# Kernel tuning notes

Measured on AMD Instinct MI355X. Metric: run time of the kernel, lower is better.

The kernel has to match this reference:

```python
import jax, jax.numpy as jnp
import numpy as np

B = 2097152   # batch
Z = 16        # z_dim
K = 64        # num_hidden_nodes


def setup_inputs() -> dict:
    key = jax.random.key(0)
    k1, k2, k3, k4, k5 = jax.random.split(key, 5)
    return {
        "z": jax.random.normal(k1, (B, Z), dtype=jnp.float32),
        "a_0": jax.random.normal(k2, (1,), dtype=jnp.float32),
        "bk": jax.random.normal(k3, (K,), dtype=jnp.float32),
        "ck": jax.random.normal(k4, (K, Z), dtype=jnp.float32),
        "dk": jax.random.normal(k5, (K,), dtype=jnp.float32),
    }


def reference(z, a_0, bk, ck, dk):
    # Vectorized over the batch: y[b] = a_0 + sum_k bk[k] * tanh((ck @ z[b])[k] + dk[k])
    h = jnp.tanh(jnp.einsum("bz,kz->bk", z, ck) + dk)  # [B, K]
    y = a_0 + h @ bk                                     # [B]
    return y[:, None]                                     # [B, 1]
```

## Files before the change

kernel.cpp:

```cpp
#include <hip/hip_runtime.h>
#include <stdint.h>

typedef __attribute__((ext_vector_type(8)))  short  short8;
typedef __attribute__((ext_vector_type(8)))  __bf16 bf16x8;
typedef __attribute__((ext_vector_type(16))) float  floatx16;
typedef __attribute__((ext_vector_type(4)))  float  floatx4;
typedef __attribute__((ext_vector_type(2)))  float  float2v;
typedef __attribute__((ext_vector_type(4)))  uint32_t uint4v;

union Frag { short8 s; bf16x8 v; uint4v d; };
union FU   { float f; uint32_t u; };

__device__ __forceinline__ short f2bf(float f) {
    FU x; x.f = f;
    uint32_t r = x.u + 0x7fffu + ((x.u >> 16) & 1u);
    return (short)(r >> 16);
}

__device__ __forceinline__ uint32_t pack_bf2(float lo, float hi) {
    FU a, b; a.f = lo; b.f = hi;
    return __builtin_amdgcn_perm(b.u + 0x8000u, a.u + 0x8000u, 0x07060302u);
}

__device__ __forceinline__ float fexp2(float x) { return __builtin_amdgcn_exp2f(x); }
__device__ __forceinline__ float frcp(float x)  { return __builtin_amdgcn_rcpf(x); }

__device__ __forceinline__ float2v tpair(float a, float b) {
    float2v t;
    t.x = fexp2(fminf(a, 15.0f));
    t.y = fexp2(fminf(b, 15.0f));
    return t + 1.0f;
}

__global__ __launch_bounds__(256, 7) void mave_kernel(
    const float* __restrict__ z,
    const float* __restrict__ a0,
    const float* __restrict__ bk,
    const float* __restrict__ ck,
    const float* __restrict__ dk,
    float* __restrict__ out,
    int ntiles)
{
    const int lane = threadIdx.x & 63;
    const int m    = lane & 31;
    const int g    = lane >> 5;
    const float S  = 2.885390081777927f;

    __shared__ __align__(16) float   cinitL[2][2][16];
    __shared__ __align__(16) float2v nbL[2][2][8];
    __shared__ float baseL;

    const int wid   = (int)((blockIdx.x * blockDim.x + threadIdx.x) >> 6);
    const int tile0 = wid * 4;
    const int tlast = ntiles - 1;

    const float* zp = z + (size_t)m * 16 + g * 8;

    floatx4 zb[2][2];
    #pragma unroll
    for (int i = 0; i < 2; ++i) {
        int ti = tile0 + i; if (ti > tlast) ti = tlast;
        const float* q = zp + (size_t)ti * 512;
        zb[i][0] = *(const floatx4*)q;
        zb[i][1] = *(const floatx4*)(q + 4);
    }

    Frag af[2];
    {
        const float* c0 = ck + m * 16 + g * 8;
        #pragma unroll
        for (int e = 0; e < 8; ++e) {
            af[0].s[e] = f2bf(c0[e] * S);
            af[1].s[e] = f2bf(c0[512 + e] * S);
        }
    }

    if (threadIdx.x < 64) {
        const int t = threadIdx.x;
        {
            const int gg = t >> 5, hh = (t >> 4) & 1, r = t & 15;
            const int n  = (r & 3) + 8 * (r >> 2) + 4 * gg + 32 * hh;
            cinitL[gg][hh][r] = S * dk[n];
        }
        if (t < 32) {
            const int gg = t >> 4, hh = (t >> 3) & 1, j = t & 7;
            const int nl = (j & 3) + 8 * (j >> 2) + 4 * gg + 32 * hh;
            float2v nb; nb.x = -2.0f * bk[nl]; nb.y = -2.0f * bk[nl + 16];
            nbL[gg][hh][j] = nb;
        }
        float bv = bk[t];
        #pragma unroll
        for (int d = 1; d < 64; d <<= 1) bv += __shfl_xor(bv, d, 64);
        if (t == 0) baseL = a0[0] + bv;
    }
    __syncthreads();

    if (tile0 >= ntiles) return;

    const floatx4* cqg = (const floatx4*)&cinitL[g][0][0];
    const floatx4* nqg = (const floatx4*)&nbL[g][0][0];

    float yv[4];
    #pragma unroll
    for (int i = 0; i < 4; ++i) {
        Frag bfr;
        bfr.d[0] = pack_bf2(zb[i & 1][0].x, zb[i & 1][0].y);
        bfr.d[1] = pack_bf2(zb[i & 1][0].z, zb[i & 1][0].w);
        bfr.d[2] = pack_bf2(zb[i & 1][1].x, zb[i & 1][1].y);
        bfr.d[3] = pack_bf2(zb[i & 1][1].z, zb[i & 1][1].w);

        if (i + 2 < 4) {
            int ti = tile0 + i + 2; if (ti > tlast) ti = tlast;
            const float* q = zp + (size_t)ti * 512;
            zb[i & 1][0] = *(const floatx4*)q;
            zb[i & 1][1] = *(const floatx4*)(q + 4);
        }

        int zz = 0;
        asm volatile("" : "+v"(zz));
        const floatx4* cq = cqg + zz;
        const floatx4* nq = nqg + zz;

        float ya = 0.0f;
        #pragma unroll
        for (int h = 0; h < 2; ++h) {
            union { floatx16 v; floatx4 q[4]; } C;
            C.q[0] = cq[h * 4 + 0]; C.q[1] = cq[h * 4 + 1];
            C.q[2] = cq[h * 4 + 2]; C.q[3] = cq[h * 4 + 3];
            floatx16 acc = __builtin_amdgcn_mfma_f32_32x32x16_bf16(
                af[h].v, bfr.v, C.v, 0, 0, 0);

            union { floatx4 q; float2v p[2]; } N0, N1, N2, N3;
            N0.q = nq[h * 4 + 0];
            N1.q = nq[h * 4 + 1];
            N2.q = nq[h * 4 + 2];
            N3.q = nq[h * 4 + 3];

            float2v T0 = tpair(acc[0], acc[8]);
            float2v T1 = tpair(acc[1], acc[9]);
            float2v P01 = T0 * T1;
            float2v n01 = N0.p[0] * T1 + N0.p[1] * T0;
            float2v T2 = tpair(acc[2], acc[10]);
            float2v T3 = tpair(acc[3], acc[11]);
            float2v P23 = T2 * T3;
            float2v n23 = N1.p[0] * T3 + N1.p[1] * T2;
            float2v T4 = tpair(acc[4], acc[12]);
            float2v T5 = tpair(acc[5], acc[13]);
            float2v P45 = T4 * T5;
            float2v n45 = N2.p[0] * T5 + N2.p[1] * T4;
            float2v T6 = tpair(acc[6], acc[14]);
            float2v T7 = tpair(acc[7], acc[15]);
            float2v P67 = T6 * T7;
            float2v n67 = N3.p[0] * T7 + N3.p[1] * T6;

            float2v PA = P01 * P23, PB = P45 * P67;
            float2v nA = n01 * P23 + n23 * P01;
            float2v nB = n45 * P67 + n67 * P45;
            float2v P  = PA * PB;
            float2v Num = nA * PB + nB * PA;
            float2v R; R.x = frcp(P.x); R.y = frcp(P.y);
            float2v Yh = Num * R;
            ya += Yh.x + Yh.y;
        }
        yv[i] = ya;
    }

    const float base = baseL;
    float ov[4];
    #pragma unroll
    for (int i = 0; i < 4; ++i) ov[i] = __shfl_xor(yv[i], 32, 64);
    if (g == 0) {
        #pragma unroll
        for (int i = 0; i < 4; ++i) {
            int ti = tile0 + i; if (ti > tlast) ti = tlast;
            out[(size_t)ti * 32 + m] = base + yv[i] + ov[i];
        }
    }
}

extern "C" void kernel_launch(void* const* d_in, const int* in_sizes, int n_in,
                              void* d_out, int out_size, void* d_ws, size_t ws_size,
                              hipStream_t stream) {
    const float* z  = (const float*)d_in[0];
    const float* a0 = (const float*)d_in[1];
    const float* bk = (const float*)d_in[2];
    const float* ck = (const float*)d_in[3];
    const float* dk = (const float*)d_in[4];
    float* out = (float*)d_out;

    const int B      = in_sizes[0] / 16;
    const int ntiles = B / 32;

    const int blocks = (ntiles + 15) / 16;
    hipLaunchKernelGGL(mave_kernel, dim3(blocks), dim3(256), 0, stream,
                       z, a0, bk, ck, dk, out, ntiles);
}
```

Measured before the change: 204.4 us.

## Give each wave private constant tables, drop block barrier, halve tiles per wave

Every wave now builds its own copy of the dk/bk-derived constant tables in shared memory and computes the bias sum itself. This removes the block-wide __syncthreads and the early-exit ordering around it. Each wave now handles two tiles instead of four, and the grid doubles to compensate. All loads, including ck, are issued up front so their latencies overlap. The cost is redundant per-wave setup work and more waves overall, with less amortization of that setup.

New measurement: 196.5 us. 3.9% less time.

```diff
diff --git a/kernel.cpp b/kernel.cpp
--- a/kernel.cpp
+++ b/kernel.cpp
@@ -44,18 +44,35 @@
     const int lane = threadIdx.x & 63;
     const int m    = lane & 31;
     const int g    = lane >> 5;
+    const int widx = threadIdx.x >> 6;
     const float S  = 2.885390081777927f;
 
-    __shared__ __align__(16) float   cinitL[2][2][16];
-    __shared__ __align__(16) float2v nbL[2][2][8];
-    __shared__ float baseL;
+    __shared__ __align__(16) float   cinitL[4][2][2][16];
+    __shared__ __align__(16) float2v nbL[4][2][2][8];
 
     const int wid   = (int)((blockIdx.x * blockDim.x + threadIdx.x) >> 6);
-    const int tile0 = wid * 4;
+    const int tile0 = wid * 2;
+    if (tile0 >= ntiles) return;
     const int tlast = ntiles - 1;
 
+    const float* c0 = ck + m * 16 + g * 8;
+    floatx4 ckv0 = *(const floatx4*)c0;
+    floatx4 ckv1 = *(const floatx4*)(c0 + 4);
+    floatx4 ckv2 = *(const floatx4*)(c0 + 512);
+    floatx4 ckv3 = *(const floatx4*)(c0 + 516);
+
+    const int tl = lane;
+    const int gg = tl >> 5, hh = (tl >> 4) & 1, rr = tl & 15;
+    const int nc = (rr & 3) + 8 * (rr >> 2) + 4 * gg + 32 * hh;
+    float dkv = dk[nc];
+    float bkt = bk[tl];
+    const int g2 = tl >> 4, h2 = (tl >> 3) & 1, j2 = tl & 7;
+    const int nl = (j2 & 3) + 8 * (j2 >> 2) + 4 * g2 + 32 * h2;
+    float bnl = 0.0f, bnh = 0.0f;
+    if (tl < 32) { bnl = bk[nl]; bnh = bk[nl + 16]; }
+    float a0v = a0[0];
+
     const float* zp = z + (size_t)m * 16 + g * 8;
-
     floatx4 zb[2][2];
     #pragma unroll
     for (int i = 0; i < 2; ++i) {
@@ -66,55 +83,35 @@
     }
 
     Frag af[2];
-    {
-        const float* c0 = ck + m * 16 + g * 8;
-        #pragma unroll
-        for (int e = 0; e < 8; ++e) {
-            af[0].s[e] = f2bf(c0[e] * S);
-            af[1].s[e] = f2bf(c0[512 + e] * S);
-        }
+    #pragma unroll
+    for (int e = 0; e < 4; ++e) {
+        af[0].s[e]     = f2bf(ckv0[e] * S);
+        af[0].s[e + 4] = f2bf(ckv1[e] * S);
+        af[1].s[e]     = f2bf(ckv2[e] * S);
+        af[1].s[e + 4] = f2bf(ckv3[e] * S);
     }
 
-    if (threadIdx.x < 64) {
-        const int t = threadIdx.x;
-        {
-            const int gg = t >> 5, hh = (t >> 4) & 1, r = t & 15;
-            const int n  = (r & 3) + 8 * (r >> 2) + 4 * gg + 32 * hh;
-            cinitL[gg][hh][r] = S * dk[n];
-        }
-        if (t < 32) {
-            const int gg = t >> 4, hh = (t >> 3) & 1, j = t & 7;
-            const int nl = (j & 3) + 8 * (j >> 2) + 4 * gg + 32 * hh;
-            float2v nb; nb.x = -2.0f * bk[nl]; nb.y = -2.0f * bk[nl + 16];
-            nbL[gg][hh][j] = nb;
-        }
-        float bv = bk[t];
-        #pragma unroll
-        for (int d = 1; d < 64; d <<= 1) bv += __shfl_xor(bv, d, 64);
-        if (t == 0) baseL = a0[0] + bv;
+    cinitL[widx][gg][hh][rr] = S * dkv;
+    if (tl < 32) {
+        float2v nb; nb.x = -2.0f * bnl; nb.y = -2.0f * bnh;
+        nbL[widx][g2][h2][j2] = nb;
     }
-    __syncthreads();
+    float bv = bkt;
+    #pragma unroll
+    for (int d = 1; d < 64; d <<= 1) bv += __shfl_xor(bv, d, 64);
+    const float base = a0v + bv;
 
-    if (tile0 >= ntiles) return;
+    const floatx4* cqg = (const floatx4*)&cinitL[widx][g][0][0];
+    const floatx4* nqg = (const floatx4*)&nbL[widx][g][0][0];
 
-    const floatx4* cqg = (const floatx4*)&cinitL[g][0][0];
-    const floatx4* nqg = (const floatx4*)&nbL[g][0][0];
-
-    float yv[4];
+    float yv[2];
     #pragma unroll
-    for (int i = 0; i < 4; ++i) {
+    for (int i = 0; i < 2; ++i) {
         Frag bfr;
-        bfr.d[0] = pack_bf2(zb[i & 1][0].x, zb[i & 1][0].y);
-        bfr.d[1] = pack_bf2(zb[i & 1][0].z, zb[i & 1][0].w);
-        bfr.d[2] = pack_bf2(zb[i & 1][1].x, zb[i & 1][1].y);
-        bfr.d[3] = pack_bf2(zb[i & 1][1].z, zb[i & 1][1].w);
-
-        if (i + 2 < 4) {
-            int ti = tile0 + i + 2; if (ti > tlast) ti = tlast;
-            const float* q = zp + (size_t)ti * 512;
-            zb[i & 1][0] = *(const floatx4*)q;
-            zb[i & 1][1] = *(const floatx4*)(q + 4);
-        }
+        bfr.d[0] = pack_bf2(zb[i][0].x, zb[i][0].y);
+        bfr.d[1] = pack_bf2(zb[i][0].z, zb[i][0].w);
+        bfr.d[2] = pack_bf2(zb[i][1].x, zb[i][1].y);
+        bfr.d[3] = pack_bf2(zb[i][1].z, zb[i][1].w);
 
         int zz = 0;
         asm volatile("" : "+v"(zz));
@@ -165,13 +162,12 @@
         yv[i] = ya;
     }
 
-    const float base = baseL;
-    float ov[4];
+    float ov[2];
     #pragma unroll
-    for (int i = 0; i < 4; ++i) ov[i] = __shfl_xor(yv[i], 32, 64);
+    for (int i = 0; i < 2; ++i) ov[i] = __shfl_xor(yv[i], 32, 64);
     if (g == 0) {
         #pragma unroll
-        for (int i = 0; i < 4; ++i) {
+        for (int i = 0; i < 2; ++i) {
             int ti = tile0 + i; if (ti > tlast) ti = tlast;
             out[(size_t)ti * 32 + m] = base + yv[i] + ov[i];
         }
@@ -191,7 +187,7 @@
     const int B      = in_sizes[0] / 16;
     const int ntiles = B / 32;
 
-    const int blocks = (ntiles + 15) / 16;
+    const int blocks = (ntiles + 7) / 8;
     hipLaunchKernelGGL(mave_kernel, dim3(blocks), dim3(256), 0, stream,
                        z, a0, bk, ck, dk, out, ntiles);
 }
```
